# Kernel optimization log

Hardware: AMD Instinct MI355X
Metric: run time of the kernel (lower is better)

## Reference

```python
import jax, jax.numpy as jnp
import numpy as np

N, IN_FEAT, LAT_FEAT, OUT_FEAT = 131072, 128, 128, 256
NUM_EXPERTS, TOP_K, OMEGA = 8, 2, 30.0


def setup_inputs() -> dict:
    key = jax.random.key(0)
    ks = jax.random.split(key, 8)
    u = lambda k_, shape, lim: jax.random.uniform(k_, shape, jnp.float32, -lim, lim)
    w_lim = np.sqrt(6.0 / IN_FEAT) / OMEGA  # SIREN init for non-first layers
    return {
        "x": jax.random.normal(ks[0], (N, IN_FEAT), jnp.float32),
        "latents": jax.random.normal(ks[1], (N, LAT_FEAT), jnp.float32),
        "gate_w": u(ks[2], (IN_FEAT, NUM_EXPERTS), 1.0 / np.sqrt(IN_FEAT)),
        "gate_b": jnp.zeros((NUM_EXPERTS,), jnp.float32),
        "W": u(ks[3], (NUM_EXPERTS, IN_FEAT, OUT_FEAT), w_lim),
        "b": u(ks[4], (NUM_EXPERTS, OUT_FEAT), 1.0 / np.sqrt(IN_FEAT)),
        "Wl": u(ks[5], (NUM_EXPERTS, LAT_FEAT, 2 * OUT_FEAT), 1.0 / np.sqrt(LAT_FEAT)),
        "bl": u(ks[6], (NUM_EXPERTS, 2 * OUT_FEAT), 1.0 / np.sqrt(LAT_FEAT)),
    }


def reference(x, latents, gate_w, gate_b, W, b, Wl, bl):
    # Gating: top-k over expert logits, softmax over the selected k logits.
    logits = x @ gate_w + gate_b                      # [N, E]
    top_vals, top_idx = jax.lax.top_k(logits, TOP_K)  # [N, k]
    top_w = jax.nn.softmax(top_vals, axis=-1)         # [N, k]
    # Dense combine weights: combine[n, e] = sum_i top_w[n, i] * (top_idx[n,i]==e).
    # Mathematically identical to the masked gather/scatter loop in torch.
    combine = jnp.sum(
        jax.nn.one_hot(top_idx, NUM_EXPERTS, dtype=x.dtype) * top_w[..., None],
        axis=1,
    )  # [N, E]
    out = jnp.zeros((x.shape[0], OUT_FEAT), x.dtype)
    for e in range(NUM_EXPERTS):  # fixed small loop over experts
        h = x @ W[e] + b[e]                    # [N, out]
        lat = latents @ Wl[e] + bl[e]          # [N, 2*out]
        scale, shift = lat[:, :OUT_FEAT], lat[:, OUT_FEAT:]
        out = out + combine[:, e:e + 1] * jnp.sin(OMEGA * h * scale + shift)
    return (out, latents)
```

## Files before the change

### kernel.cpp

```cpp
#include <hip/hip_runtime.h>

#define INF_  128
#define OUTF  256
#define LATF  128
#define OUT2  512
#define NEXP  8
#define OMEGA_ 30.0f

typedef float  f32x4  __attribute__((ext_vector_type(4)));
typedef __bf16 bf16x8 __attribute__((ext_vector_type(8)));
typedef unsigned short ushort8 __attribute__((ext_vector_type(8)));

#define PACK_THREADS (NEXP * 4 * 4 * 3 * 4 * 64)
#define EXP_STRIDE   (4 * 4 * 3 * 4 * 512)
#define PH_STRIDE    6144
#define GEMM_COMPUTE 1056
#define COPY_BLOCKS  512
#define GEMM_GRID    (GEMM_COMPUTE + COPY_BLOCKS)
#define CAP          131072

__device__ __forceinline__ unsigned short bfbits(float f) {
    unsigned int u = __builtin_bit_cast(unsigned int, f);
    return (unsigned short)((u + 0x7FFFu + ((u >> 16) & 1u)) >> 16);
}

__device__ __forceinline__ bf16x8 cvt8(f32x4 a, f32x4 b) {
    bf16x8 r;
    r[0] = (__bf16)a.x; r[1] = (__bf16)a.y; r[2] = (__bf16)a.z; r[3] = (__bf16)a.w;
    r[4] = (__bf16)b.x; r[5] = (__bf16)b.y; r[6] = (__bf16)b.z; r[7] = (__bf16)b.w;
    return r;
}

__device__ __forceinline__ f32x4 bload(const unsigned short* p) {
    const ushort4 u = *(const ushort4*)p;
    f32x4 r;
    r.x = __builtin_bit_cast(float, (unsigned int)u.x << 16);
    r.y = __builtin_bit_cast(float, (unsigned int)u.y << 16);
    r.z = __builtin_bit_cast(float, (unsigned int)u.z << 16);
    r.w = __builtin_bit_cast(float, (unsigned int)u.w << 16);
    return r;
}

#define GLOAD_LDS16(g, l) __builtin_amdgcn_global_load_lds( \
    (const __attribute__((address_space(1))) unsigned int*)(g), \
    (__attribute__((address_space(3))) unsigned int*)(l), 16, 0, 0)

__global__ void prep_kernel(const float* __restrict__ x,
                            const float* __restrict__ gw,
                            const float* __restrict__ gb,
                            const float* __restrict__ W,
                            const float* __restrict__ Wl,
                            unsigned int* __restrict__ cur,
                            unsigned int* __restrict__ perm,
                            float2* __restrict__ wps,
                            unsigned short* __restrict__ Bpk,
                            int nGate)
{
    __shared__ float sgw[INF_ * NEXP];
    __shared__ int lc[64];
    __shared__ unsigned int lbase[64];
    const int tid = threadIdx.x;

    if ((int)blockIdx.x >= nGate) {
        const int t = ((int)blockIdx.x - nGate) * 256 + tid;
        if (t >= PACK_THREADS) return;
        const int l   = t & 63;
        const int ks  = (t >> 6) & 3;
        const int m3  = (t >> 8) % 3;
        const int g   = (t >> 8) / 3;
        const int nf  = g & 3, nc = (g >> 2) & 3, e = g >> 4;
        const int col = nc * 64 + nf * 16 + (l & 15);
        const int kb  = ks * 32 + (l >> 4) * 8;
        ushort8 o;
#pragma unroll
        for (int j = 0; j < 8; ++j) {
            float v;
            if (m3 == 0) v = W [((size_t)e * 128 + kb + j) * 256 + col];
            else         v = Wl[((size_t)e * 128 + kb + j) * 512 + col + (m3 == 2 ? 256 : 0)];
            o[j] = bfbits(v);
        }
        *(ushort8*)(Bpk + (size_t)t * 8) = o;
        return;
    }

    ((float4*)sgw)[tid] = ((const float4*)gw)[tid];
    if (tid < 64) lc[tid] = 0;
    __syncthreads();

    const int t = blockIdx.x * 256 + tid;
    float acc[8];
#pragma unroll
    for (int e = 0; e < 8; ++e) acc[e] = gb[e];
    const float4* xr = (const float4*)(x + (size_t)t * INF_);
#pragma unroll 8
    for (int i = 0; i < 32; ++i) {
        float4 v = xr[i];
#pragma unroll
        for (int j = 0; j < 4; ++j) {
            const float xk = (&v.x)[j];
            const float4 g0 = *(const float4*)&sgw[(i * 4 + j) * 8];
            const float4 g1 = *(const float4*)&sgw[(i * 4 + j) * 8 + 4];
            acc[0] += xk * g0.x; acc[1] += xk * g0.y; acc[2] += xk * g0.z; acc[3] += xk * g0.w;
            acc[4] += xk * g1.x; acc[5] += xk * g1.y; acc[6] += xk * g1.z; acc[7] += xk * g1.w;
        }
    }
    float best = -1e30f, sec = -1e30f; int bi = 0, si = 0;
#pragma unroll
    for (int e = 0; e < 8; ++e) {
        const float v = acc[e];
        if (v > best)      { sec = best; si = bi; best = v; bi = e; }
        else if (v > sec)  { sec = v; si = e; }
    }
    const float ew  = __expf(sec - best);
    const float inv = 1.0f / (1.0f + ew);
    const float wb  = inv, wsc = ew * inv;
    int emin, emax; float wmin, wmax;
    if (bi < si) { emin = bi; wmin = wb;  emax = si; wmax = wsc; }
    else         { emin = si; wmin = wsc; emax = bi; wmax = wb;  }
    const int pid = emin * 8 + emax;

    const int p = atomicAdd(&lc[pid], 1);
    __syncthreads();
    if (tid < 64) { lbase[tid] = lc[tid] ? atomicAdd(&cur[tid], (unsigned int)lc[tid]) : 0u; }
    __syncthreads();
    const size_t q = (size_t)pid * CAP + lbase[pid] + (unsigned int)p;
    perm[q] = (unsigned int)t;
    wps[q]  = make_float2(wmin, wmax);
}

__launch_bounds__(256, 3)
__global__ void moe_gemm_kernel(const float* __restrict__ x,
                                const float* __restrict__ lat,
                                const unsigned short* __restrict__ Bpk,
                                const float* __restrict__ bias,
                                const float* __restrict__ biasl,
                                const unsigned int* __restrict__ c,
                                const unsigned int* __restrict__ perm,
                                const float2* __restrict__ wps,
                                float* __restrict__ out,
                                float* __restrict__ lat_out)
{
    __shared__ __align__(16) unsigned short sB[2][2 * PH_STRIDE];
    __shared__ __align__(16) unsigned short sbias[6 * 256];

    const unsigned int dd = blockIdx.x;
    const int tid  = threadIdx.x;

    if (dd >= GEMM_COMPUTE) {
        const int cb = (int)dd - GEMM_COMPUTE;
        const f32x4* src = (const f32x4*)lat + (size_t)cb * 8192;
        f32x4*       dst = (f32x4*)lat_out   + (size_t)cb * 8192;
#pragma unroll
        for (int i = 0; i < 32; ++i) {
            f32x4 v = __builtin_nontemporal_load(&src[tid + i * 256]);
            __builtin_nontemporal_store(v, &dst[tid + i * 256]);
        }
        return;
    }

    const unsigned int bid = (dd & 7) * (GEMM_COMPUTE / 8) + (dd >> 3);
    const int lane = tid & 63;

    const unsigned int n_l  = c[lane];
    const unsigned int nt_l = (n_l + 127) >> 7;
    unsigned int ts = nt_l;
#pragma unroll
    for (int s = 1; s < 64; s <<= 1) {
        unsigned int tt = __shfl_up(ts, s);
        if (lane >= s) ts += tt;
    }
    const unsigned int texcl  = ts - nt_l;
    const unsigned int ntiles = __shfl(ts, 63);
    if (bid >= ntiles) return;
    const unsigned long long mk = __ballot(bid >= texcl);
    const int pid  = __popcll(mk) - 1;
    const int tile = (int)(bid - __shfl(texcl, pid));
    const unsigned int cn = __shfl(n_l, pid);
    const int emin = pid >> 3, emax = pid & 7;
    const int rows = min(128, (int)(cn - (unsigned int)tile * 128u));
    const unsigned int* permS = perm + (size_t)pid * CAP + (size_t)tile * 128u;
    const float2* wS = wps + (size_t)pid * CAP + (size_t)tile * 128u;

    const int w    = tid >> 6;
    const int lrow = lane & 15;
    const int lgrp = lane >> 4;
    const int half = tid >> 7;
    const int wh   = (tid >> 6) & 1;
    const int t7   = tid & 127;

    const int r0 = w * 32 + lrow, r1 = r0 + 16;
    const int t0 = (int)permS[min(r0, rows - 1)];
    const int t1 = (int)permS[min(r1, rows - 1)];
    const float2 w0 = wS[min(r0, rows - 1)];
    const float2 w1 = wS[min(r1, rows - 1)];
    bf16x8 ax[2][4], al[2][4];
    {
        const float* x0 = x   + (size_t)t0 * INF_;
        const float* x1 = x   + (size_t)t1 * INF_;
        const float* l0 = lat + (size_t)t0 * LATF;
        const float* l1 = lat + (size_t)t1 * LATF;
#pragma unroll
        for (int ks = 0; ks < 4; ++ks) {
            const int kb = ks * 32 + lgrp * 8;
            ax[0][ks] = cvt8(__builtin_nontemporal_load((const f32x4*)(x0 + kb)),
                             __builtin_nontemporal_load((const f32x4*)(x0 + kb + 4)));
            ax[1][ks] = cvt8(__builtin_nontemporal_load((const f32x4*)(x1 + kb)),
                             __builtin_nontemporal_load((const f32x4*)(x1 + kb + 4)));
            al[0][ks] = cvt8(__builtin_nontemporal_load((const f32x4*)(l0 + kb)),
                             __builtin_nontemporal_load((const f32x4*)(l0 + kb + 4)));
            al[1][ks] = cvt8(__builtin_nontemporal_load((const f32x4*)(l1 + kb)),
                             __builtin_nontemporal_load((const f32x4*)(l1 + kb + 4)));
        }
    }

    const unsigned short* B0 = Bpk + (size_t)emin * EXP_STRIDE;
    const unsigned short* B1 = Bpk + (size_t)emax * EXP_STRIDE;
    const unsigned short* Bh = half ? B1 : B0;

    {
        const int i4 = (tid & 63) * 4;
        const int sg = tid >> 6;
#pragma unroll
        for (int rep = 0; rep < 2; ++rep) {
            const int seg = sg + rep * 4;
            if (seg < 6) {
                const float* bsrc =
                    (seg == 0) ? bias  + emin * OUTF :
                    (seg == 1) ? bias  + emax * OUTF :
                    (seg == 2) ? biasl + emin * OUT2 :
                    (seg == 3) ? biasl + emin * OUT2 + 256 :
                    (seg == 4) ? biasl + emax * OUT2 :
                                 biasl + emax * OUT2 + 256;
                const f32x4 v = *(const f32x4*)(bsrc + i4);
                ushort4 u;
                u.x = bfbits(v.x); u.y = bfbits(v.y); u.z = bfbits(v.z); u.w = bfbits(v.w);
                *(ushort4*)&sbias[seg * 256 + i4] = u;
            }
        }
    }

    auto STAGE = [&](int ph, int buf) {
        const unsigned short* src = Bh + (size_t)ph * PH_STRIDE + (size_t)t7 * 8;
        unsigned short* dst = &sB[buf][half * PH_STRIDE + wh * 512];
#pragma unroll
        for (int r = 0; r < 6; ++r)
            GLOAD_LDS16(src + r * 1024, dst + r * 1024);
    };

    f32x4 acc[2][3][2];
    auto COMPUTE = [&](int buf) {
#pragma unroll
        for (int ex = 0; ex < 2; ++ex)
#pragma unroll
            for (int m = 0; m < 3; ++m)
#pragma unroll
                for (int mf = 0; mf < 2; ++mf) acc[ex][m][mf] = (f32x4)0.0f;
#pragma unroll
        for (int ex = 0; ex < 2; ++ex) {
#pragma unroll
            for (int m = 0; m < 3; ++m) {
                bf16x8 bb[4];
#pragma unroll
                for (int ks = 0; ks < 4; ++ks)
                    bb[ks] = *(const bf16x8*)&sB[buf][ex * PH_STRIDE + (m * 4 + ks) * 512 + lane * 8];
#pragma unroll
                for (int ks = 0; ks < 4; ++ks) {
#pragma unroll
                    for (int mf = 0; mf < 2; ++mf) {
                        const bf16x8 a = (m == 0) ? ax[mf][ks] : al[mf][ks];
                        acc[ex][m][mf] = __builtin_amdgcn_mfma_f32_16x16x32_bf16(bb[ks], a, acc[ex][m][mf], 0, 0, 0);
                    }
                }
            }
        }
    };

    auto EPILOGUE = [&](int ph, bool guard) {
        const int cb = ph * 16 + lgrp * 4;
        const f32x4 b0h = bload(&sbias[0 * 256 + cb]);
        const f32x4 b1h = bload(&sbias[1 * 256 + cb]);
        const f32x4 b0s = bload(&sbias[2 * 256 + cb]);
        const f32x4 b0f = bload(&sbias[3 * 256 + cb]);
        const f32x4 b1s = bload(&sbias[4 * 256 + cb]);
        const f32x4 b1f = bload(&sbias[5 * 256 + cb]);
#pragma unroll
        for (int mf = 0; mf < 2; ++mf) {
            const int  rr  = mf ? r1 : r0;
            if (guard && rr >= rows) continue;
            const int  tok = mf ? t1 : t0;
            const float wmn = mf ? w1.x : w0.x;
            const float wmx = mf ? w1.y : w0.y;
            f32x4 v;
#pragma unroll
            for (int j = 0; j < 4; ++j) {
                const float h0 = acc[0][0][mf][j] + b0h[j];
                const float s0 = acc[0][1][mf][j] + b0s[j];
                const float f0 = acc[0][2][mf][j] + b0f[j];
                const float h1 = acc[1][0][mf][j] + b1h[j];
                const float s1 = acc[1][1][mf][j] + b1s[j];
                const float f1 = acc[1][2][mf][j] + b1f[j];
                v[j] = wmn * __sinf(OMEGA_ * h0 * s0 + f0)
                     + wmx * __sinf(OMEGA_ * h1 * s1 + f1);
            }
            *(f32x4*)(out + (size_t)tok * OUTF + cb) = v;
        }
    };

    STAGE(0, 0);
    asm volatile("s_waitcnt vmcnt(0) lgkmcnt(0)" ::: "memory");
    __builtin_amdgcn_s_barrier();
    __builtin_amdgcn_sched_barrier(0);

    if (rows == 128) {
#pragma unroll 1
        for (int ph = 0; ph < 16; ++ph) {
            const int buf = ph & 1;
            if (ph < 15) STAGE(ph + 1, buf ^ 1);
            COMPUTE(buf);
            EPILOGUE(ph, false);
            __builtin_amdgcn_sched_barrier(0);
            if (ph < 15) {
                asm volatile("s_waitcnt vmcnt(2)" ::: "memory");
                __builtin_amdgcn_s_barrier();
                __builtin_amdgcn_sched_barrier(0);
            }
        }
    } else {
#pragma unroll 1
        for (int ph = 0; ph < 16; ++ph) {
            const int buf = ph & 1;
            if (ph > 0) {
                STAGE(ph, buf);
                asm volatile("s_waitcnt vmcnt(0)" ::: "memory");
                __builtin_amdgcn_s_barrier();
                __builtin_amdgcn_sched_barrier(0);
            }
            COMPUTE(buf);
            EPILOGUE(ph, true);
            __builtin_amdgcn_s_barrier();
            __builtin_amdgcn_sched_barrier(0);
        }
    }
}

extern "C" void kernel_launch(void* const* d_in, const int* in_sizes, int n_in,
                              void* d_out, int out_size, void* d_ws, size_t ws_size,
                              hipStream_t stream)
{
    const float* x   = (const float*)d_in[0];
    const float* lat = (const float*)d_in[1];
    const float* gw  = (const float*)d_in[2];
    const float* gb  = (const float*)d_in[3];
    const float* W   = (const float*)d_in[4];
    const float* b   = (const float*)d_in[5];
    const float* Wl  = (const float*)d_in[6];
    const float* bl  = (const float*)d_in[7];
    float* out = (float*)d_out;
    const int N = in_sizes[0] / INF_;

    char* ws = (char*)d_ws;
    unsigned int*   cur  = (unsigned int*)ws;
    unsigned short* Bpk  = (unsigned short*)(ws + 4096);
    unsigned int*   perm = (unsigned int*)(ws + (4096 + 2 * (size_t)EXP_STRIDE * NEXP + 4096));
    float2*         wps  = (float2*)((char*)perm + (size_t)64 * CAP * sizeof(unsigned int));

    (void)hipMemsetAsync(cur, 0, 256, stream);

    const int nGate = N / 256;
    prep_kernel<<<dim3(nGate + PACK_THREADS / 256), 256, 0, stream>>>(
        x, gw, gb, W, Wl, cur, perm, wps, Bpk, nGate);

    moe_gemm_kernel<<<dim3(GEMM_GRID), 256, 0, stream>>>(
        x, lat, Bpk, b, bl, cur, perm, wps, out, out + (size_t)N * OUTF);
}
```

Baseline: 146.0 us.

## Enlarge MoE GEMM row tile to 192 with six waves per block

```diff
diff --git a/kernel.cpp b/kernel.cpp
--- a/kernel.cpp
+++ b/kernel.cpp
@@ -14,7 +14,8 @@
 #define PACK_THREADS (NEXP * 4 * 4 * 3 * 4 * 64)
 #define EXP_STRIDE   (4 * 4 * 3 * 4 * 512)
 #define PH_STRIDE    6144
-#define GEMM_COMPUTE 1056
+#define TILE_M       192
+#define GEMM_COMPUTE 752
 #define COPY_BLOCKS  512
 #define GEMM_GRID    (GEMM_COMPUTE + COPY_BLOCKS)
 #define CAP          131072
@@ -128,7 +129,7 @@
     wps[q]  = make_float2(wmin, wmax);
 }
 
-__launch_bounds__(256, 3)
+__launch_bounds__(384, 3)
 __global__ void moe_gemm_kernel(const float* __restrict__ x,
                                 const float* __restrict__ lat,
                                 const unsigned short* __restrict__ Bpk,
@@ -150,10 +151,9 @@
         const int cb = (int)dd - GEMM_COMPUTE;
         const f32x4* src = (const f32x4*)lat + (size_t)cb * 8192;
         f32x4*       dst = (f32x4*)lat_out   + (size_t)cb * 8192;
-#pragma unroll
-        for (int i = 0; i < 32; ++i) {
-            f32x4 v = __builtin_nontemporal_load(&src[tid + i * 256]);
-            __builtin_nontemporal_store(v, &dst[tid + i * 256]);
+        for (int i = tid; i < 8192; i += 384) {
+            f32x4 v = __builtin_nontemporal_load(&src[i]);
+            __builtin_nontemporal_store(v, &dst[i]);
         }
         return;
     }
@@ -162,7 +162,7 @@
     const int lane = tid & 63;
 
     const unsigned int n_l  = c[lane];
-    const unsigned int nt_l = (n_l + 127) >> 7;
+    const unsigned int nt_l = (n_l + (TILE_M - 1)) / TILE_M;
     unsigned int ts = nt_l;
 #pragma unroll
     for (int s = 1; s < 64; s <<= 1) {
@@ -177,16 +177,15 @@
     const int tile = (int)(bid - __shfl(texcl, pid));
     const unsigned int cn = __shfl(n_l, pid);
     const int emin = pid >> 3, emax = pid & 7;
-    const int rows = min(128, (int)(cn - (unsigned int)tile * 128u));
-    const unsigned int* permS = perm + (size_t)pid * CAP + (size_t)tile * 128u;
-    const float2* wS = wps + (size_t)pid * CAP + (size_t)tile * 128u;
+    const int rows = min(TILE_M, (int)(cn - (unsigned int)tile * TILE_M));
+    const unsigned int* permS = perm + (size_t)pid * CAP + (size_t)tile * TILE_M;
+    const float2* wS = wps + (size_t)pid * CAP + (size_t)tile * TILE_M;
 
     const int w    = tid >> 6;
     const int lrow = lane & 15;
     const int lgrp = lane >> 4;
-    const int half = tid >> 7;
-    const int wh   = (tid >> 6) & 1;
-    const int t7   = tid & 127;
+    const int half = (w >= 3) ? 1 : 0;
+    const int wh   = w - half * 3;
 
     const int r0 = w * 32 + lrow, r1 = r0 + 16;
     const int t0 = (int)permS[min(r0, rows - 1)];
@@ -218,33 +217,27 @@
     const unsigned short* Bh = half ? B1 : B0;
 
     {
-        const int i4 = (tid & 63) * 4;
-        const int sg = tid >> 6;
-#pragma unroll
-        for (int rep = 0; rep < 2; ++rep) {
-            const int seg = sg + rep * 4;
-            if (seg < 6) {
-                const float* bsrc =
-                    (seg == 0) ? bias  + emin * OUTF :
-                    (seg == 1) ? bias  + emax * OUTF :
-                    (seg == 2) ? biasl + emin * OUT2 :
-                    (seg == 3) ? biasl + emin * OUT2 + 256 :
-                    (seg == 4) ? biasl + emax * OUT2 :
-                                 biasl + emax * OUT2 + 256;
-                const f32x4 v = *(const f32x4*)(bsrc + i4);
-                ushort4 u;
-                u.x = bfbits(v.x); u.y = bfbits(v.y); u.z = bfbits(v.z); u.w = bfbits(v.w);
-                *(ushort4*)&sbias[seg * 256 + i4] = u;
-            }
-        }
+        const int i4 = lane * 4;
+        const int seg = w;
+        const float* bsrc =
+            (seg == 0) ? bias  + emin * OUTF :
+            (seg == 1) ? bias  + emax * OUTF :
+            (seg == 2) ? biasl + emin * OUT2 :
+            (seg == 3) ? biasl + emin * OUT2 + 256 :
+            (seg == 4) ? biasl + emax * OUT2 :
+                         biasl + emax * OUT2 + 256;
+        const f32x4 v = *(const f32x4*)(bsrc + i4);
+        ushort4 u;
+        u.x = bfbits(v.x); u.y = bfbits(v.y); u.z = bfbits(v.z); u.w = bfbits(v.w);
+        *(ushort4*)&sbias[seg * 256 + i4] = u;
     }
 
     auto STAGE = [&](int ph, int buf) {
-        const unsigned short* src = Bh + (size_t)ph * PH_STRIDE + (size_t)t7 * 8;
-        unsigned short* dst = &sB[buf][half * PH_STRIDE + wh * 512];
-#pragma unroll
-        for (int r = 0; r < 6; ++r)
-            GLOAD_LDS16(src + r * 1024, dst + r * 1024);
+        const unsigned short* src = Bh + (size_t)ph * PH_STRIDE + wh * 2048 + lane * 8;
+        unsigned short* dst = &sB[buf][half * PH_STRIDE + wh * 2048];
+#pragma unroll
+        for (int r = 0; r < 4; ++r)
+            GLOAD_LDS16(src + r * 512, dst + r * 512);
     };
 
     f32x4 acc[2][3][2];
@@ -311,7 +304,7 @@
     __builtin_amdgcn_s_barrier();
     __builtin_amdgcn_sched_barrier(0);
 
-    if (rows == 128) {
+    if (rows == TILE_M) {
 #pragma unroll 1
         for (int ph = 0; ph < 16; ++ph) {
             const int buf = ph & 1;
@@ -370,6 +363,6 @@
     prep_kernel<<<dim3(nGate + PACK_THREADS / 256), 256, 0, stream>>>(
         x, gw, gb, W, Wl, cur, perm, wps, Bpk, nGate);
 
-    moe_gemm_kernel<<<dim3(GEMM_GRID), 256, 0, stream>>>(
+    moe_gemm_kernel<<<dim3(GEMM_GRID), 384, 0, stream>>>(
         x, lat, Bpk, b, bl, cur, perm, wps, out, out + (size_t)N * OUTF);
 }
```

Measured after the change: 181.4 us. +24.2%, slower.

## Single-buffer LDS staging to raise occupancy from 3 to 5 blocks per CU

Applied to the files above, without the earlier changes.

```diff
diff --git a/kernel.cpp b/kernel.cpp
--- a/kernel.cpp
+++ b/kernel.cpp
@@ -128,7 +128,7 @@
     wps[q]  = make_float2(wmin, wmax);
 }
 
-__launch_bounds__(256, 3)
+__launch_bounds__(256, 5)
 __global__ void moe_gemm_kernel(const float* __restrict__ x,
                                 const float* __restrict__ lat,
                                 const unsigned short* __restrict__ Bpk,
@@ -140,7 +140,7 @@
                                 float* __restrict__ out,
                                 float* __restrict__ lat_out)
 {
-    __shared__ __align__(16) unsigned short sB[2][2 * PH_STRIDE];
+    __shared__ __align__(16) unsigned short sB[2 * PH_STRIDE];
     __shared__ __align__(16) unsigned short sbias[6 * 256];
 
     const unsigned int dd = blockIdx.x;
@@ -239,16 +239,16 @@
         }
     }
 
-    auto STAGE = [&](int ph, int buf) {
+    auto STAGE = [&](int ph) {
         const unsigned short* src = Bh + (size_t)ph * PH_STRIDE + (size_t)t7 * 8;
-        unsigned short* dst = &sB[buf][half * PH_STRIDE + wh * 512];
+        unsigned short* dst = &sB[half * PH_STRIDE + wh * 512];
 #pragma unroll
         for (int r = 0; r < 6; ++r)
             GLOAD_LDS16(src + r * 1024, dst + r * 1024);
     };
 
     f32x4 acc[2][3][2];
-    auto COMPUTE = [&](int buf) {
+    auto COMPUTE = [&]() {
 #pragma unroll
         for (int ex = 0; ex < 2; ++ex)
 #pragma unroll
@@ -262,7 +262,7 @@
                 bf16x8 bb[4];
 #pragma unroll
                 for (int ks = 0; ks < 4; ++ks)
-                    bb[ks] = *(const bf16x8*)&sB[buf][ex * PH_STRIDE + (m * 4 + ks) * 512 + lane * 8];
+                    bb[ks] = *(const bf16x8*)&sB[ex * PH_STRIDE + (m * 4 + ks) * 512 + lane * 8];
 #pragma unroll
                 for (int ks = 0; ks < 4; ++ks) {
 #pragma unroll
@@ -306,37 +306,22 @@
         }
     };
 
-    STAGE(0, 0);
+    STAGE(0);
     asm volatile("s_waitcnt vmcnt(0) lgkmcnt(0)" ::: "memory");
     __builtin_amdgcn_s_barrier();
     __builtin_amdgcn_sched_barrier(0);
 
-    if (rows == 128) {
+    const bool guard = (rows != 128);
 #pragma unroll 1
-        for (int ph = 0; ph < 16; ++ph) {
-            const int buf = ph & 1;
-            if (ph < 15) STAGE(ph + 1, buf ^ 1);
-            COMPUTE(buf);
-            EPILOGUE(ph, false);
-            __builtin_amdgcn_sched_barrier(0);
-            if (ph < 15) {
-                asm volatile("s_waitcnt vmcnt(2)" ::: "memory");
-                __builtin_amdgcn_s_barrier();
-                __builtin_amdgcn_sched_barrier(0);
-            }
-        }
-    } else {
-#pragma unroll 1
-        for (int ph = 0; ph < 16; ++ph) {
-            const int buf = ph & 1;
-            if (ph > 0) {
-                STAGE(ph, buf);
-                asm volatile("s_waitcnt vmcnt(0)" ::: "memory");
-                __builtin_amdgcn_s_barrier();
-                __builtin_amdgcn_sched_barrier(0);
-            }
-            COMPUTE(buf);
-            EPILOGUE(ph, true);
+    for (int ph = 0; ph < 16; ++ph) {
+        COMPUTE();
+        EPILOGUE(ph, guard);
+        __builtin_amdgcn_sched_barrier(0);
+        __builtin_amdgcn_s_barrier();
+        __builtin_amdgcn_sched_barrier(0);
+        if (ph < 15) {
+            STAGE(ph + 1);
+            asm volatile("s_waitcnt vmcnt(0)" ::: "memory");
             __builtin_amdgcn_s_barrier();
             __builtin_amdgcn_sched_barrier(0);
         }
```

After: 415.0 us. 184% more time.
